# Performance work log

Measured on AMD Instinct MI355X. Metric: run time of the kernel, lower is better.

## Reference

```python
import jax, jax.numpy as jnp
import numpy as np

B = 256        # number of graphs (batch * num_choices)
H = 128        # conv_hidden
N = 262144     # total nodes across all graphs (~1024 nodes/graph)


def setup_inputs() -> dict:
    key = jax.random.key(0)
    k1, k2, k3, k4 = jax.random.split(key, 4)
    s = jax.random.normal(k1, (B, H), dtype=jnp.float32)            # x1: one query per graph
    node_embeds = jax.random.normal(k2, (N, H), dtype=jnp.float32)  # ragged node features, flat
    weight = jax.random.normal(k3, (H, H), dtype=jnp.float32) / np.float32(np.sqrt(H))
    segment_ids = jnp.sort(jax.random.randint(k4, (N,), 0, B))      # node -> graph id (sorted, like dgl batching)
    return {"s": s, "node_embeds": node_embeds, "weight": weight, "segment_ids": segment_ids}


def reference(s, node_embeds, weight, segment_ids):
    # Per-graph attention pooling, vectorized over all graphs at once.
    # Original per-graph: h = (nodes @ W) . s_i ; sh = softmax(h) ; pooled = sh @ nodes
    num_segments = s.shape[0]
    h_proj = node_embeds @ weight                          # [N, H]
    h = jnp.einsum('nh,nh->n', h_proj, s[segment_ids])    # [N] per-node score
    # segment-wise stable softmax
    m = jax.ops.segment_max(h, segment_ids, num_segments=num_segments)      # [B]
    e = jnp.exp(h - m[segment_ids])                                          # [N]
    denom = jax.ops.segment_sum(e, segment_ids, num_segments=num_segments)  # [B]
    sh = e / denom[segment_ids]                                              # [N]
    pooled = jax.ops.segment_sum(sh[:, None] * node_embeds, segment_ids,
                                 num_segments=num_segments)                  # [B, H]
    return pooled
```

## Files before the change

kernel.cpp:

```cpp
#include <hip/hip_runtime.h>
#include <math.h>

#define HDIM 128
#define SENT -1e30f
#define DEPTH 8

__device__ __forceinline__ int wave_lower_bound(const int* __restrict__ seg, int N, int target) {
    const int lane = threadIdx.x & 63;
    int lo = 0, hi = N;
    while (hi - lo > 64) {
        int len = hi - lo;
        int chunk = (len + 63) >> 6;
        int pos = lo + lane * chunk;
        int v = (pos < hi) ? seg[pos] : 0x7fffffff;
        unsigned long long bal = __ballot(v < target);
        int cnt = __popcll(bal);
        if (cnt == 0) { hi = lo; break; }
        int nlo = lo + (cnt - 1) * chunk + 1;
        int nhi = (cnt < 64) ? min(hi, lo + cnt * chunk) : hi;
        lo = nlo; hi = nhi;
    }
    int pos = lo + lane;
    int v = (pos < hi) ? seg[pos] : 0x7fffffff;
    unsigned long long bal = __ballot(v < target);
    return lo + __popcll(bal);
}

__global__ void __launch_bounds__(1024, 4)
att_pool_kernel(const float* __restrict__ s,
                const float* __restrict__ x,
                const float* __restrict__ W,
                const int*   __restrict__ seg,
                float*       __restrict__ out,
                int N, int B)
{
    const int b    = blockIdx.x;
    const int tid  = threadIdx.x;
    const int wave = tid >> 6;
    const int lane = tid & 63;
    const int half = lane >> 5;
    const int hl   = lane & 31;

    __shared__ float ws_lds[HDIM];
    __shared__ int   se[2];
    __shared__ float lm[32], ll[32];
    __shared__ float lacc[32][HDIM];
    __shared__ float sscale[32];
    __shared__ float sdenom;

    if (wave == 0) {
        int v = wave_lower_bound(seg, N, b);
        if (lane == 0) se[0] = v;
    } else if (wave == 1) {
        int v = wave_lower_bound(seg, N, b + 1);
        if (lane == 0) se[1] = v;
    } else if (wave < 10) {
        const int k = (wave - 2) * 16 + (lane >> 2);
        const int g = lane & 3;
        const float* Wr = W + (size_t)k * HDIM;
        const float* sr = s + (size_t)b * HDIM;
        float partial = 0.f;
        #pragma unroll
        for (int ii = 0; ii < 8; ++ii) {
            int j0 = (g + 4 * ii) * 4;
            float4 wv4 = *reinterpret_cast<const float4*>(Wr + j0);
            float4 sv4 = *reinterpret_cast<const float4*>(sr + j0);
            partial += wv4.x * sv4.x + wv4.y * sv4.y + wv4.z * sv4.z + wv4.w * sv4.w;
        }
        partial += __shfl_xor(partial, 1, 64);
        partial += __shfl_xor(partial, 2, 64);
        if (g == 0) ws_lds[k] = partial;
    }
    __syncthreads();

    const int start = se[0];
    const int end   = se[1];
    const int last  = end - 1;
    const float4 wv = *reinterpret_cast<const float4*>(&ws_lds[4 * hl]);

    float  m = SENT, l = 0.f;
    float4 acc = make_float4(0.f, 0.f, 0.f, 0.f);

    for (int p = start; p < end; p += 16 * DEPTH * 2) {
        const int rb = p + 2 * DEPTH * wave + half;

        float4 xv[DEPTH];
        #pragma unroll
        for (int k = 0; k < DEPTH; ++k) {
            const int c = min(rb + 2 * k, last);
            xv[k] = *reinterpret_cast<const float4*>(x + (size_t)c * HDIM + 4 * hl);
        }

        float h[DEPTH];
        #pragma unroll
        for (int k = 0; k < DEPTH; ++k)
            h[k] = xv[k].x * wv.x + xv[k].y * wv.y + xv[k].z * wv.z + xv[k].w * wv.w;

        #pragma unroll
        for (int off = 16; off >= 1; off >>= 1) {
            #pragma unroll
            for (int k = 0; k < DEPTH; ++k) h[k] += __shfl_xor(h[k], off, 64);
        }

        float mn = m;
        #pragma unroll
        for (int k = 0; k < DEPTH; ++k) {
            h[k] = (rb + 2 * k < end) ? h[k] : SENT;
            mn = fmaxf(mn, h[k]);
        }

        float sc = __expf(m - mn);
        float e[DEPTH];
        float esum = 0.f;
        #pragma unroll
        for (int k = 0; k < DEPTH; ++k) {
            e[k] = (rb + 2 * k < end) ? __expf(h[k] - mn) : 0.f;
            esum += e[k];
        }

        float ax = acc.x * sc, ay = acc.y * sc, az = acc.z * sc, aw = acc.w * sc;
        #pragma unroll
        for (int k = 0; k < DEPTH; ++k) {
            ax += e[k] * xv[k].x;
            ay += e[k] * xv[k].y;
            az += e[k] * xv[k].z;
            aw += e[k] * xv[k].w;
        }
        acc = make_float4(ax, ay, az, aw);
        l = l * sc + esum;
        m = mn;
    }

    const int st = wave * 2 + half;
    *reinterpret_cast<float4*>(&lacc[st][4 * hl]) = acc;
    if (hl == 0) { lm[st] = m; ll[st] = l; }
    __syncthreads();

    if (wave == 0 && lane < 32) {
        float mi = lm[lane], li = ll[lane];
        float M = mi;
        #pragma unroll
        for (int off = 16; off >= 1; off >>= 1) M = fmaxf(M, __shfl_xor(M, off, 64));
        float sc = (li > 0.f) ? __expf(mi - M) : 0.f;
        float d  = li * sc;
        #pragma unroll
        for (int off = 16; off >= 1; off >>= 1) d += __shfl_xor(d, off, 64);
        sscale[lane] = sc;
        if (lane == 0) sdenom = d;
    }
    __syncthreads();

    if (tid < HDIM) {
        float num = 0.f;
        #pragma unroll
        for (int i = 0; i < 32; ++i) num += lacc[i][tid] * sscale[i];
        float D = sdenom;
        out[(size_t)b * HDIM + tid] = (D > 0.f) ? (num / D) : 0.f;
    }
}

extern "C" void kernel_launch(void* const* d_in, const int* in_sizes, int n_in,
                              void* d_out, int out_size, void* d_ws, size_t ws_size,
                              hipStream_t stream) {
    const float* s   = (const float*)d_in[0];
    const float* x   = (const float*)d_in[1];
    const float* W   = (const float*)d_in[2];
    const int*   seg = (const int*)  d_in[3];
    float* out = (float*)d_out;

    const int B = in_sizes[0] / HDIM;
    const int N = in_sizes[3];

    att_pool_kernel<<<B, 1024, 0, stream>>>(s, x, W, seg, out, N, B);
}
```

Baseline: 32.72 us.

## Split per-graph pooling into prep, split-segment partial, and merge kernels

Replaces the single 1024-thread-per-graph kernel with three launches. The first precomputes W·s and the segment bounds, the second splits each graph's nodes across 8 smaller 256-thread blocks that run an online softmax with double-buffered loads, and the third merges the partial max, sum and accumulator records. The aim is more, smaller blocks that balance load across CUs and overlap memory traffic better. In exchange it adds two extra launches and a workspace round trip for the partials.

```diff
diff --git a/kernel.cpp b/kernel.cpp
--- a/kernel.cpp
+++ b/kernel.cpp
@@ -3,7 +3,8 @@
 
 #define HDIM 128
 #define SENT -1e30f
-#define DEPTH 8
+#define CPG  8
+#define RECF 132
 
 __device__ __forceinline__ int wave_lower_bound(const int* __restrict__ seg, int N, int target) {
     const int lane = threadIdx.x & 63;
@@ -26,109 +27,127 @@
     return lo + __popcll(bal);
 }
 
-__global__ void __launch_bounds__(1024, 4)
-att_pool_kernel(const float* __restrict__ s,
-                const float* __restrict__ x,
-                const float* __restrict__ W,
-                const int*   __restrict__ seg,
-                float*       __restrict__ out,
-                int N, int B)
+__global__ void __launch_bounds__(384)
+k_prep(const float* __restrict__ s, const float* __restrict__ W,
+       const int* __restrict__ seg, float* __restrict__ wsw,
+       int* __restrict__ bounds, int N, int B)
 {
-    const int b    = blockIdx.x;
+    const int b = blockIdx.x;
+    const int wave = threadIdx.x >> 6;
+    const int lane = threadIdx.x & 63;
+    if (wave < 4) {
+        const int k = wave * 32 + (lane >> 1);
+        const int g = lane & 1;
+        const float* Wr = W + (size_t)k * HDIM + g * 64;
+        const float* sr = s + (size_t)b * HDIM + g * 64;
+        float p = 0.f;
+        #pragma unroll
+        for (int ii = 0; ii < 16; ++ii) {
+            float4 wv4 = *reinterpret_cast<const float4*>(Wr + 4 * ii);
+            float4 sv4 = *reinterpret_cast<const float4*>(sr + 4 * ii);
+            p += wv4.x * sv4.x + wv4.y * sv4.y + wv4.z * sv4.z + wv4.w * sv4.w;
+        }
+        p += __shfl_xor(p, 1, 64);
+        if (g == 0) wsw[(size_t)b * HDIM + k] = p;
+    } else if (wave == 4) {
+        int v = wave_lower_bound(seg, N, b);
+        if (lane == 0) bounds[b] = v;
+    } else {
+        if (b == B - 1 && lane == 0) bounds[B] = N;
+    }
+}
+
+__global__ void __launch_bounds__(256, 6)
+k_partial(const float* __restrict__ x, const float* __restrict__ wsw,
+          const int* __restrict__ bounds, float* __restrict__ partials)
+{
+    const int gblk = blockIdx.x;
+    const int b    = gblk >> 3;
+    const int j    = gblk & (CPG - 1);
     const int tid  = threadIdx.x;
     const int wave = tid >> 6;
     const int lane = tid & 63;
     const int half = lane >> 5;
     const int hl   = lane & 31;
 
-    __shared__ float ws_lds[HDIM];
-    __shared__ int   se[2];
-    __shared__ float lm[32], ll[32];
-    __shared__ float lacc[32][HDIM];
-    __shared__ float sscale[32];
-    __shared__ float sdenom;
-
-    if (wave == 0) {
-        int v = wave_lower_bound(seg, N, b);
-        if (lane == 0) se[0] = v;
-    } else if (wave == 1) {
-        int v = wave_lower_bound(seg, N, b + 1);
-        if (lane == 0) se[1] = v;
-    } else if (wave < 10) {
-        const int k = (wave - 2) * 16 + (lane >> 2);
-        const int g = lane & 3;
-        const float* Wr = W + (size_t)k * HDIM;
-        const float* sr = s + (size_t)b * HDIM;
-        float partial = 0.f;
-        #pragma unroll
-        for (int ii = 0; ii < 8; ++ii) {
-            int j0 = (g + 4 * ii) * 4;
-            float4 wv4 = *reinterpret_cast<const float4*>(Wr + j0);
-            float4 sv4 = *reinterpret_cast<const float4*>(sr + j0);
-            partial += wv4.x * sv4.x + wv4.y * sv4.y + wv4.z * sv4.z + wv4.w * sv4.w;
-        }
-        partial += __shfl_xor(partial, 1, 64);
-        partial += __shfl_xor(partial, 2, 64);
-        if (g == 0) ws_lds[k] = partial;
-    }
+    __shared__ __align__(16) float ws_lds[HDIM];
+    __shared__ __align__(16) float lacc[8][HDIM];
+    __shared__ float lm[8], ll[8], sscale[8];
+    __shared__ float sM, sL;
+
+    if (tid < 32)
+        reinterpret_cast<float4*>(ws_lds)[tid] =
+            reinterpret_cast<const float4*>(wsw + (size_t)b * HDIM)[tid];
     __syncthreads();
 
-    const int start = se[0];
-    const int end   = se[1];
-    const int last  = end - 1;
-    const float4 wv = *reinterpret_cast<const float4*>(&ws_lds[4 * hl]);
+    const int s0 = bounds[b];
+    const int e0 = bounds[b + 1];
+    const int len = e0 - s0;
+    const int lo = s0 + ((len * j) >> 3);
+    const int hi = s0 + ((len * (j + 1)) >> 3);
+
+    const float4 wv = *reinterpret_cast<const float4*>(ws_lds + 4 * hl);
+    const float* xb = x + 4 * hl;
 
     float  m = SENT, l = 0.f;
     float4 acc = make_float4(0.f, 0.f, 0.f, 0.f);
 
-    for (int p = start; p < end; p += 16 * DEPTH * 2) {
-        const int rb = p + 2 * DEPTH * wave + half;
-
-        float4 xv[DEPTH];
-        #pragma unroll
-        for (int k = 0; k < DEPTH; ++k) {
-            const int c = min(rb + 2 * k, last);
-            xv[k] = *reinterpret_cast<const float4*>(x + (size_t)c * HDIM + 4 * hl);
+    if (lo < hi) {
+        const int lastc = hi - 1;
+        const int rbase = 8 * wave + half;
+
+        float4 A0, A1, A2, A3, B0, B1, B2, B3;
+
+        #define LOAD(d0,d1,d2,d3, pp) do {                                        \
+            int r0_ = (pp) + rbase,     c0_ = min(r0_, lastc);                    \
+            int r1_ = (pp) + rbase + 2, c1_ = min(r1_, lastc);                    \
+            int r2_ = (pp) + rbase + 4, c2_ = min(r2_, lastc);                    \
+            int r3_ = (pp) + rbase + 6, c3_ = min(r3_, lastc);                    \
+            d0 = *reinterpret_cast<const float4*>(xb + (size_t)c0_ * HDIM);       \
+            d1 = *reinterpret_cast<const float4*>(xb + (size_t)c1_ * HDIM);       \
+            d2 = *reinterpret_cast<const float4*>(xb + (size_t)c2_ * HDIM);       \
+            d3 = *reinterpret_cast<const float4*>(xb + (size_t)c3_ * HDIM);       \
+        } while (0)
+
+        #define PROC(d0,d1,d2,d3, pp) do {                                        \
+            float h0 = d0.x*wv.x + d0.y*wv.y + d0.z*wv.z + d0.w*wv.w;             \
+            float h1 = d1.x*wv.x + d1.y*wv.y + d1.z*wv.z + d1.w*wv.w;             \
+            float h2 = d2.x*wv.x + d2.y*wv.y + d2.z*wv.z + d2.w*wv.w;             \
+            float h3 = d3.x*wv.x + d3.y*wv.y + d3.z*wv.z + d3.w*wv.w;             \
+            _Pragma("unroll")                                                     \
+            for (int off = 16; off >= 1; off >>= 1) {                             \
+                h0 += __shfl_xor(h0, off, 64);                                    \
+                h1 += __shfl_xor(h1, off, 64);                                    \
+                h2 += __shfl_xor(h2, off, 64);                                    \
+                h3 += __shfl_xor(h3, off, 64);                                    \
+            }                                                                     \
+            const bool v0 = (pp) + rbase     < hi, v1 = (pp) + rbase + 2 < hi;    \
+            const bool v2 = (pp) + rbase + 4 < hi, v3 = (pp) + rbase + 6 < hi;    \
+            h0 = v0 ? h0 : SENT; h1 = v1 ? h1 : SENT;                             \
+            h2 = v2 ? h2 : SENT; h3 = v3 ? h3 : SENT;                             \
+            float mn = fmaxf(fmaxf(fmaxf(fmaxf(m, h0), h1), h2), h3);             \
+            float sc = __expf(m - mn);                                            \
+            float e0_ = v0 ? __expf(h0 - mn) : 0.f;                               \
+            float e1_ = v1 ? __expf(h1 - mn) : 0.f;                               \
+            float e2_ = v2 ? __expf(h2 - mn) : 0.f;                               \
+            float e3_ = v3 ? __expf(h3 - mn) : 0.f;                               \
+            l = l * sc + ((e0_ + e1_) + (e2_ + e3_));                             \
+            acc.x = acc.x*sc + e0_*d0.x + e1_*d1.x + e2_*d2.x + e3_*d3.x;         \
+            acc.y = acc.y*sc + e0_*d0.y + e1_*d1.y + e2_*d2.y + e3_*d3.y;         \
+            acc.z = acc.z*sc + e0_*d0.z + e1_*d1.z + e2_*d2.z + e3_*d3.z;         \
+            acc.w = acc.w*sc + e0_*d0.w + e1_*d1.w + e2_*d2.w + e3_*d3.w;         \
+            m = mn;                                                               \
+        } while (0)
+
+        LOAD(A0,A1,A2,A3, lo);
+        for (int p = lo; p < hi; p += 64) {
+            LOAD(B0,B1,B2,B3, p + 32);
+            PROC(A0,A1,A2,A3, p);
+            LOAD(A0,A1,A2,A3, p + 64);
+            if (p + 32 < hi) PROC(B0,B1,B2,B3, p + 32);
         }
-
-        float h[DEPTH];
-        #pragma unroll
-        for (int k = 0; k < DEPTH; ++k)
-            h[k] = xv[k].x * wv.x + xv[k].y * wv.y + xv[k].z * wv.z + xv[k].w * wv.w;
-
-        #pragma unroll
-        for (int off = 16; off >= 1; off >>= 1) {
-            #pragma unroll
-            for (int k = 0; k < DEPTH; ++k) h[k] += __shfl_xor(h[k], off, 64);
-        }
-
-        float mn = m;
-        #pragma unroll
-        for (int k = 0; k < DEPTH; ++k) {
-            h[k] = (rb + 2 * k < end) ? h[k] : SENT;
-            mn = fmaxf(mn, h[k]);
-        }
-
-        float sc = __expf(m - mn);
-        float e[DEPTH];
-        float esum = 0.f;
-        #pragma unroll
-        for (int k = 0; k < DEPTH; ++k) {
-            e[k] = (rb + 2 * k < end) ? __expf(h[k] - mn) : 0.f;
-            esum += e[k];
-        }
-
-        float ax = acc.x * sc, ay = acc.y * sc, az = acc.z * sc, aw = acc.w * sc;
-        #pragma unroll
-        for (int k = 0; k < DEPTH; ++k) {
-            ax += e[k] * xv[k].x;
-            ay += e[k] * xv[k].y;
-            az += e[k] * xv[k].z;
-            aw += e[k] * xv[k].w;
-        }
-        acc = make_float4(ax, ay, az, aw);
-        l = l * sc + esum;
-        m = mn;
+        #undef LOAD
+        #undef PROC
     }
 
     const int st = wave * 2 + half;
@@ -136,27 +155,54 @@
     if (hl == 0) { lm[st] = m; ll[st] = l; }
     __syncthreads();
 
-    if (wave == 0 && lane < 32) {
+    if (wave == 0 && lane < 8) {
         float mi = lm[lane], li = ll[lane];
         float M = mi;
-        #pragma unroll
-        for (int off = 16; off >= 1; off >>= 1) M = fmaxf(M, __shfl_xor(M, off, 64));
+        M = fmaxf(M, __shfl_xor(M, 1, 64));
+        M = fmaxf(M, __shfl_xor(M, 2, 64));
+        M = fmaxf(M, __shfl_xor(M, 4, 64));
         float sc = (li > 0.f) ? __expf(mi - M) : 0.f;
         float d  = li * sc;
-        #pragma unroll
-        for (int off = 16; off >= 1; off >>= 1) d += __shfl_xor(d, off, 64);
+        d += __shfl_xor(d, 1, 64);
+        d += __shfl_xor(d, 2, 64);
+        d += __shfl_xor(d, 4, 64);
         sscale[lane] = sc;
-        if (lane == 0) sdenom = d;
+        if (lane == 0) { sM = M; sL = d; }
     }
     __syncthreads();
 
+    float* rec = partials + (size_t)gblk * RECF;
     if (tid < HDIM) {
         float num = 0.f;
         #pragma unroll
-        for (int i = 0; i < 32; ++i) num += lacc[i][tid] * sscale[i];
-        float D = sdenom;
-        out[(size_t)b * HDIM + tid] = (D > 0.f) ? (num / D) : 0.f;
-    }
+        for (int i = 0; i < 8; ++i) num += lacc[i][tid] * sscale[i];
+        rec[4 + tid] = num;
+    } else if (tid == 128) {
+        rec[0] = sM; rec[1] = sL;
+    }
+}
+
+__global__ void __launch_bounds__(128)
+k_merge(const float* __restrict__ partials, float* __restrict__ out)
+{
+    const int b = blockIdx.x;
+    const int t = threadIdx.x;
+    float mi[CPG], li[CPG];
+    float M = SENT;
+    #pragma unroll
+    for (int i = 0; i < CPG; ++i) {
+        const float* rec = partials + (size_t)(b * CPG + i) * RECF;
+        mi[i] = rec[0]; li[i] = rec[1];
+        M = fmaxf(M, mi[i]);
+    }
+    float D = 0.f, num = 0.f;
+    #pragma unroll
+    for (int i = 0; i < CPG; ++i) {
+        float sc = (li[i] > 0.f) ? __expf(mi[i] - M) : 0.f;
+        D   += li[i] * sc;
+        num += partials[(size_t)(b * CPG + i) * RECF + 4 + t] * sc;
+    }
+    out[(size_t)b * HDIM + t] = (D > 0.f) ? (num / D) : 0.f;
 }
 
 extern "C" void kernel_launch(void* const* d_in, const int* in_sizes, int n_in,
@@ -171,5 +217,12 @@
     const int B = in_sizes[0] / HDIM;
     const int N = in_sizes[3];
 
-    att_pool_kernel<<<B, 1024, 0, stream>>>(s, x, W, seg, out, N, B);
-}
+    float* wsf      = (float*)d_ws;
+    float* wsw      = wsf;
+    float* partials = wsf + (size_t)B * HDIM;
+    int*   bounds   = (int*)(partials + (size_t)B * CPG * RECF);
+
+    k_prep   <<<B,       384, 0, stream>>>(s, W, seg, wsw, bounds, N, B);
+    k_partial<<<B * CPG, 256, 0, stream>>>(x, wsw, bounds, partials);
+    k_merge  <<<B,       128, 0, stream>>>(partials, out);
+}
```

Measured after the change: 35.34 us. 1.08x slower.
